# Optimization experiments

Hardware: AMD Instinct MI355X
Metric: run time of the kernel (lower is better)

Reference implementation:

```python
import jax, jax.numpy as jnp
import numpy as np

B, LC, LQ, D = 256, 400, 50, 128
NEG = 1e12


def setup_inputs() -> dict:
    key = jax.random.key(0)
    ks = jax.random.split(key, 7)
    return {
        "x_cont": jax.random.normal(ks[0], (B, LC, D), dtype=jnp.float32),
        "x_ques": jax.random.normal(ks[1], (B, LQ, D), dtype=jnp.float32),
        "W0": jax.random.normal(ks[2], (D, 1), dtype=jnp.float32) * (1.0 / np.sqrt(D)),
        "W1": jax.random.normal(ks[3], (D, 1), dtype=jnp.float32) * (1.0 / np.sqrt(D)),
        "W2": jax.random.normal(ks[4], (1, 1, D), dtype=jnp.float32) * (1.0 / np.sqrt(D)),
        "cont_len": jax.random.randint(ks[5], (B, 1), 1, LC, dtype=jnp.int32),
        "ques_len": jax.random.randint(ks[6], (B, 1), 1, LQ, dtype=jnp.int32),
    }


def reference(x_cont, x_ques, W0, W1, W2, cont_len, ques_len):
    # Trilinear similarity S[b,c,q] = xc.W0 + xq.W1 + (xc*W2).xq
    s_c = x_cont @ W0                                   # (B, LC, 1)
    s_q = jnp.swapaxes(x_ques @ W1, 1, 2)               # (B, 1, LQ)
    s_f = jnp.einsum('bcd,bqd->bcq', x_cont * W2, x_ques)
    S = s_c + s_q + s_f                                 # (B, LC, LQ)

    # Length masks: position valid iff pos < seq_len (matches one_hot+cumsum)
    q_mask = (jnp.arange(LQ)[None, :] < ques_len).astype(S.dtype)  # (B, LQ)
    c_mask = (jnp.arange(LC)[None, :] < cont_len).astype(S.dtype)  # (B, LC)

    S_bar = jax.nn.softmax(S - (1.0 - q_mask)[:, None, :] * NEG, axis=-1)
    S_T = jnp.swapaxes(
        jax.nn.softmax(S - (1.0 - c_mask)[:, :, None] * NEG, axis=1), 1, 2)  # (B, LQ, LC)

    c2q = S_bar @ x_ques                                # (B, LC, D)
    q2c = (S_bar @ S_T) @ x_cont                        # (B, LC, D)

    result = jnp.concatenate(
        [x_cont, c2q, x_cont * c2q, x_cont * q2c], axis=-1)  # (B, LC, 4D)
    return result, S_bar, S_T
```

## Files before the change

kernel.cpp:

```cpp
#include <hip/hip_runtime.h>
#include <math.h>

#define B 256
#define LC 400
#define LQ 50
#define D 128

#define CT 64
__global__ __launch_bounds__(256) void k_scores(
    const float* __restrict__ xc_g, const float* __restrict__ xq_g,
    const float* __restrict__ W0, const float* __restrict__ W1,
    const float* __restrict__ W2, float* __restrict__ S_raw)
{
    __shared__ __align__(16) float xq[56 * 132];
    __shared__ __align__(16) float xc[CT * 132];
    __shared__ float w[3 * D];
    __shared__ float sc[CT], sq[64];
    __shared__ float sS[CT * 51];

    const int b = blockIdx.y;
    const int c0 = blockIdx.x * CT;
    const int t = threadIdx.x;
    const int nc = min(CT, LC - c0);

    const float* xqb = xq_g + b * LQ * D;
    for (int i = t; i < LQ * D; i += 256) xq[(i >> 7) * 132 + (i & 127)] = xqb[i];
    const float* xcb = xc_g + (size_t)(b * LC + c0) * D;
    for (int i = t; i < nc * D; i += 256) xc[(i >> 7) * 132 + (i & 127)] = xcb[i];
    if (t < D) { w[t] = W0[t]; w[D + t] = W1[t]; w[2 * D + t] = W2[t]; }
    __syncthreads();

    if (t < nc) {
        const float4* r = (const float4*)(xc + t * 132);
        float4 a = {0.f, 0.f, 0.f, 0.f};
        const float4* wv = (const float4*)w;
        for (int d = 0; d < D / 4; ++d) {
            float4 u = r[d], vv = wv[d];
            a.x += u.x * vv.x; a.y += u.y * vv.y; a.z += u.z * vv.z; a.w += u.w * vv.w;
        }
        sc[t] = a.x + a.y + a.z + a.w;
    } else if (t >= 64 && t < 64 + LQ) {
        const int q = t - 64;
        const float4* r = (const float4*)(xq + q * 132);
        const float4* wv = (const float4*)(w + D);
        float4 a = {0.f, 0.f, 0.f, 0.f};
        for (int d = 0; d < D / 4; ++d) {
            float4 u = r[d], vv = wv[d];
            a.x += u.x * vv.x; a.y += u.y * vv.y; a.z += u.z * vv.z; a.w += u.w * vv.w;
        }
        sq[q] = a.x + a.y + a.z + a.w;
    }
    __syncthreads();
    for (int i = t; i < nc * D; i += 256) xc[(i >> 7) * 132 + (i & 127)] *= w[2 * D + (i & 127)];
    __syncthreads();

    const int qg = t & 7, cg = t >> 3;
    const int cA = cg * 2;
    if (cA < nc) {
        float accA[7] = {0, 0, 0, 0, 0, 0, 0};
        float accB[7] = {0, 0, 0, 0, 0, 0, 0};
        const float4* xc4 = (const float4*)xc;
        const float4* xq4 = (const float4*)xq;
#pragma unroll 8
        for (int d4 = 0; d4 < 32; ++d4) {
            const float4 a0 = xc4[cA * 33 + d4];
            const float4 a1 = xc4[(cA + 1) * 33 + d4];
#pragma unroll
            for (int j = 0; j < 7; ++j) {
                const float4 bq = xq4[(qg * 7 + j) * 33 + d4];
                accA[j] += a0.x * bq.x + a0.y * bq.y + a0.z * bq.z + a0.w * bq.w;
                accB[j] += a1.x * bq.x + a1.y * bq.y + a1.z * bq.z + a1.w * bq.w;
            }
        }
#pragma unroll
        for (int j = 0; j < 7; ++j) {
            const int q = qg * 7 + j;
            if (q < LQ) {
                sS[cA * 51 + q] = accA[j];
                sS[(cA + 1) * 51 + q] = accB[j];
            }
        }
    }
    __syncthreads();

    float* Sb = S_raw + (size_t)(b * LC + c0) * LQ;
    for (int i = t; i < nc * LQ; i += 256) {
        const int c = i / LQ, q = i % LQ;
        Sb[i] = sS[c * 51 + q] + sc[c] + sq[q];
    }
}

__global__ __launch_bounds__(512) void k_softmax_fused(
    float* S_inout, const int* __restrict__ cont_len,
    const int* __restrict__ ques_len, float* __restrict__ S_T)
{
    __shared__ float sS[LC * 53];
    __shared__ float red[512];
    __shared__ float colmax[64], colinv[64];
    __shared__ float rowmax[LC], rowinv[LC];

    const int b = blockIdx.x;
    const int t = threadIdx.x;
    const int clen = cont_len[b];
    const int qlen = ques_len[b];
    float* Sb = S_inout + (size_t)b * LC * LQ;

    for (int i = t; i < LC * LQ; i += 512) sS[(i / LQ) * 53 + (i % LQ)] = Sb[i];
    __syncthreads();

    const int q = t % LQ, r = t / LQ;
    if (r < 10) {
        float m = -INFINITY;
        const int cend = min((r + 1) * 40, clen);
        for (int c = r * 40; c < cend; ++c) m = fmaxf(m, sS[c * 53 + q]);
        red[r * LQ + q] = m;
    }
    __syncthreads();
    if (t < LQ) {
        float m = red[t];
        for (int rr = 1; rr < 10; ++rr) m = fmaxf(m, red[rr * LQ + t]);
        colmax[t] = m;
    }
    __syncthreads();
    if (r < 10) {
        float s = 0.f;
        const float cm = colmax[q];
        const int cend = min((r + 1) * 40, clen);
        for (int c = r * 40; c < cend; ++c) s += __expf(sS[c * 53 + q] - cm);
        red[r * LQ + q] = s;
    }
    __syncthreads();
    if (t < LQ) {
        float s = 0.f;
        for (int rr = 0; rr < 10; ++rr) s += red[rr * LQ + t];
        colinv[t] = 1.f / s;
    }
    if (t < LC) {
        float m = -INFINITY;
        for (int qq = 0; qq < qlen; ++qq) m = fmaxf(m, sS[t * 53 + qq]);
        float s = 0.f;
        for (int qq = 0; qq < qlen; ++qq) s += __expf(sS[t * 53 + qq] - m);
        rowmax[t] = m;
        rowinv[t] = 1.f / s;
    }
    __syncthreads();

    for (int i = t; i < LC * LQ; i += 512) {
        const int c = i / LQ, qq = i % LQ;
        const float v = (qq < qlen) ? __expf(sS[c * 53 + qq] - rowmax[c]) * rowinv[c] : 0.f;
        Sb[i] = v;
    }
    float* STb = S_T + (size_t)b * LQ * LC;
    for (int i = t; i < LQ * LC; i += 512) {
        const int qq = i / LC, c = i % LC;
        const float v = (c < clen) ? __expf(sS[c * 53 + qq] - colmax[qq]) * colinv[qq] : 0.f;
        STb[i] = v;
    }
}

__global__ __launch_bounds__(256) void k_qc(
    const float* __restrict__ S_T, const float* __restrict__ xc_g,
    float* __restrict__ T)
{
    __shared__ __align__(16) float sT[56 * 404];

    const int b = blockIdx.x;
    const int t = threadIdx.x;
    const float* STb = S_T + (size_t)b * LQ * LC;
    for (int i = t; i < LQ * LC; i += 256) sT[(i / LC) * 404 + (i % LC)] = STb[i];
    __syncthreads();

    const int d4 = t & 31, qg = t >> 5;
    float4 acc[7];
#pragma unroll
    for (int j = 0; j < 7; ++j) acc[j] = make_float4(0.f, 0.f, 0.f, 0.f);

    const float4* xcv = (const float4*)xc_g + (size_t)b * LC * 32 + d4;
    const float4* sT4 = (const float4*)sT;
    for (int c = 0; c < LC; c += 4) {
        const float4 x0 = xcv[(c + 0) * 32];
        const float4 x1 = xcv[(c + 1) * 32];
        const float4 x2 = xcv[(c + 2) * 32];
        const float4 x3 = xcv[(c + 3) * 32];
#pragma unroll
        for (int j = 0; j < 7; ++j) {
            const float4 wv = sT4[(qg * 7 + j) * 101 + (c >> 2)];
            acc[j].x += wv.x * x0.x + wv.y * x1.x + wv.z * x2.x + wv.w * x3.x;
            acc[j].y += wv.x * x0.y + wv.y * x1.y + wv.z * x2.y + wv.w * x3.y;
            acc[j].z += wv.x * x0.z + wv.y * x1.z + wv.z * x2.z + wv.w * x3.z;
            acc[j].w += wv.x * x0.w + wv.y * x1.w + wv.z * x2.w + wv.w * x3.w;
        }
    }
    float4* Tb = (float4*)T + (size_t)b * LQ * 32 + d4;
#pragma unroll
    for (int j = 0; j < 7; ++j) {
        const int qq = qg * 7 + j;
        if (qq < LQ) Tb[qq * 32] = acc[j];
    }
}

__global__ __launch_bounds__(256) void k_out(
    const float* __restrict__ S_bar, const float* __restrict__ xq_g,
    const float* __restrict__ Tm, const float* __restrict__ xc_g,
    float* __restrict__ out)
{
    __shared__ __align__(16) float xqL[LQ * 132];
    __shared__ __align__(16) float TL[LQ * 132];
    __shared__ float sbL[CT * 51];

    const int b = blockIdx.y;
    const int c0 = blockIdx.x * CT;
    const int t = threadIdx.x;
    const int nc = min(CT, LC - c0);

    const float* xqb = xq_g + (size_t)b * LQ * D;
    const float* Tb = Tm + (size_t)b * LQ * D;
    for (int i = t; i < LQ * D; i += 256) {
        xqL[(i >> 7) * 132 + (i & 127)] = xqb[i];
        TL[(i >> 7) * 132 + (i & 127)] = Tb[i];
    }
    const float* sb_g = S_bar + (size_t)(b * LC + c0) * LQ;
    for (int i = t; i < nc * LQ; i += 256) sbL[(i / LQ) * 51 + (i % LQ)] = sb_g[i];
    __syncthreads();

    const int d4 = t & 31, cg = t >> 5;
    float4 c2q[8], q2c[8];
#pragma unroll
    for (int i = 0; i < 8; ++i) {
        c2q[i] = make_float4(0.f, 0.f, 0.f, 0.f);
        q2c[i] = make_float4(0.f, 0.f, 0.f, 0.f);
    }
    const float4* xq4 = (const float4*)xqL;
    const float4* T4 = (const float4*)TL;
    const int cbase = cg * 8;
    for (int qq = 0; qq < LQ; ++qq) {
        const float4 xv = xq4[qq * 33 + d4];
        const float4 tv = T4[qq * 33 + d4];
#pragma unroll
        for (int i = 0; i < 8; ++i) {
            const float wq = sbL[(cbase + i) * 51 + qq];
            c2q[i].x += wq * xv.x; c2q[i].y += wq * xv.y;
            c2q[i].z += wq * xv.z; c2q[i].w += wq * xv.w;
            q2c[i].x += wq * tv.x; q2c[i].y += wq * tv.y;
            q2c[i].z += wq * tv.z; q2c[i].w += wq * tv.w;
        }
    }

    const float4* xcv = (const float4*)xc_g;
    float4* out4 = (float4*)out;
#pragma unroll
    for (int i = 0; i < 8; ++i) {
        const int c = cbase + i;
        if (c < nc) {
            const int row = b * LC + c0 + c;
            const float4 xc = xcv[(size_t)row * 32 + d4];
            float4* o = out4 + (size_t)row * 128 + d4;
            o[0] = xc;
            o[32] = c2q[i];
            o[64] = make_float4(xc.x * c2q[i].x, xc.y * c2q[i].y,
                                xc.z * c2q[i].z, xc.w * c2q[i].w);
            o[96] = make_float4(xc.x * q2c[i].x, xc.y * q2c[i].y,
                                xc.z * q2c[i].z, xc.w * q2c[i].w);
        }
    }
}

extern "C" void kernel_launch(void* const* d_in, const int* in_sizes, int n_in,
                              void* d_out, int out_size, void* d_ws, size_t ws_size,
                              hipStream_t stream)
{
    (void)in_sizes; (void)n_in; (void)out_size; (void)ws_size;
    const float* x_cont = (const float*)d_in[0];
    const float* x_ques = (const float*)d_in[1];
    const float* W0 = (const float*)d_in[2];
    const float* W1 = (const float*)d_in[3];
    const float* W2 = (const float*)d_in[4];
    const int* cont_len = (const int*)d_in[5];
    const int* ques_len = (const int*)d_in[6];

    float* out = (float*)d_out;
    float* out_res  = out;
    float* out_Sbar = out + (size_t)B * LC * 4 * D;
    float* out_ST   = out_Sbar + (size_t)B * LC * LQ;
    float* Tws = (float*)d_ws;

    k_scores<<<dim3(7, B), 256, 0, stream>>>(x_cont, x_ques, W0, W1, W2, out_Sbar);
    k_softmax_fused<<<B, 512, 0, stream>>>(out_Sbar, cont_len, ques_len, out_ST);
    k_qc<<<B, 256, 0, stream>>>(out_ST, x_cont, Tws);
    k_out<<<dim3(7, B), 256, 0, stream>>>(out_Sbar, x_ques, Tws, x_cont, out_res);
}
```

Measured before the change: 439.8 us.

## Fuse score computation with softmax into one per-batch kernel and vectorize loads

Merges the score kernel and the softmax kernel into a single block per batch. It tiles over context rows in shared memory and prefetches the next tile into registers, so raw scores never round-trip through global memory and one launch is removed. The W2 scaling moves from the context rows to the question matrix. It also vectorizes the S_T staging load in k_qc and transposes S_bar in shared memory in k_out so weights can be read as float4. The trade-off is much less grid parallelism for the score stage (256 blocks, only half the threads doing the main product) and higher shared-memory use per block.

```diff
diff --git a/kernel.cpp b/kernel.cpp
--- a/kernel.cpp
+++ b/kernel.cpp
@@ -5,156 +5,184 @@
 #define LC 400
 #define LQ 50
 #define D 128
-
 #define CT 64
-__global__ __launch_bounds__(256) void k_scores(
+
+__global__ __launch_bounds__(256) void k_scores_softmax(
     const float* __restrict__ xc_g, const float* __restrict__ xq_g,
     const float* __restrict__ W0, const float* __restrict__ W1,
-    const float* __restrict__ W2, float* __restrict__ S_raw)
+    const float* __restrict__ W2, const int* __restrict__ cont_len,
+    const int* __restrict__ ques_len,
+    float* __restrict__ S_bar, float* __restrict__ S_T)
 {
+    __shared__ float sS[LC * 51];
     __shared__ __align__(16) float xq[56 * 132];
-    __shared__ __align__(16) float xc[CT * 132];
+    __shared__ __align__(16) float xc[64 * 132];
     __shared__ float w[3 * D];
-    __shared__ float sc[CT], sq[64];
-    __shared__ float sS[CT * 51];
-
-    const int b = blockIdx.y;
-    const int c0 = blockIdx.x * CT;
-    const int t = threadIdx.x;
-    const int nc = min(CT, LC - c0);
-
-    const float* xqb = xq_g + b * LQ * D;
-    for (int i = t; i < LQ * D; i += 256) xq[(i >> 7) * 132 + (i & 127)] = xqb[i];
-    const float* xcb = xc_g + (size_t)(b * LC + c0) * D;
-    for (int i = t; i < nc * D; i += 256) xc[(i >> 7) * 132 + (i & 127)] = xcb[i];
-    if (t < D) { w[t] = W0[t]; w[D + t] = W1[t]; w[2 * D + t] = W2[t]; }
-    __syncthreads();
-
-    if (t < nc) {
-        const float4* r = (const float4*)(xc + t * 132);
-        float4 a = {0.f, 0.f, 0.f, 0.f};
-        const float4* wv = (const float4*)w;
-        for (int d = 0; d < D / 4; ++d) {
-            float4 u = r[d], vv = wv[d];
-            a.x += u.x * vv.x; a.y += u.y * vv.y; a.z += u.z * vv.z; a.w += u.w * vv.w;
-        }
-        sc[t] = a.x + a.y + a.z + a.w;
-    } else if (t >= 64 && t < 64 + LQ) {
-        const int q = t - 64;
-        const float4* r = (const float4*)(xq + q * 132);
-        const float4* wv = (const float4*)(w + D);
-        float4 a = {0.f, 0.f, 0.f, 0.f};
-        for (int d = 0; d < D / 4; ++d) {
-            float4 u = r[d], vv = wv[d];
-            a.x += u.x * vv.x; a.y += u.y * vv.y; a.z += u.z * vv.z; a.w += u.w * vv.w;
-        }
-        sq[q] = a.x + a.y + a.z + a.w;
-    }
-    __syncthreads();
-    for (int i = t; i < nc * D; i += 256) xc[(i >> 7) * 132 + (i & 127)] *= w[2 * D + (i & 127)];
-    __syncthreads();
-
-    const int qg = t & 7, cg = t >> 3;
-    const int cA = cg * 2;
-    if (cA < nc) {
-        float accA[7] = {0, 0, 0, 0, 0, 0, 0};
-        float accB[7] = {0, 0, 0, 0, 0, 0, 0};
-        const float4* xc4 = (const float4*)xc;
-        const float4* xq4 = (const float4*)xq;
-#pragma unroll 8
-        for (int d4 = 0; d4 < 32; ++d4) {
-            const float4 a0 = xc4[cA * 33 + d4];
-            const float4 a1 = xc4[(cA + 1) * 33 + d4];
-#pragma unroll
-            for (int j = 0; j < 7; ++j) {
-                const float4 bq = xq4[(qg * 7 + j) * 33 + d4];
-                accA[j] += a0.x * bq.x + a0.y * bq.y + a0.z * bq.z + a0.w * bq.w;
-                accB[j] += a1.x * bq.x + a1.y * bq.y + a1.z * bq.z + a1.w * bq.w;
-            }
-        }
-#pragma unroll
-        for (int j = 0; j < 7; ++j) {
-            const int q = qg * 7 + j;
-            if (q < LQ) {
-                sS[cA * 51 + q] = accA[j];
-                sS[(cA + 1) * 51 + q] = accB[j];
-            }
-        }
-    }
-    __syncthreads();
-
-    float* Sb = S_raw + (size_t)(b * LC + c0) * LQ;
-    for (int i = t; i < nc * LQ; i += 256) {
-        const int c = i / LQ, q = i % LQ;
-        Sb[i] = sS[c * 51 + q] + sc[c] + sq[q];
-    }
-}
-
-__global__ __launch_bounds__(512) void k_softmax_fused(
-    float* S_inout, const int* __restrict__ cont_len,
-    const int* __restrict__ ques_len, float* __restrict__ S_T)
-{
-    __shared__ float sS[LC * 53];
-    __shared__ float red[512];
-    __shared__ float colmax[64], colinv[64];
+    __shared__ float scT[64];
+    __shared__ float sq[56];
     __shared__ float rowmax[LC], rowinv[LC];
+    __shared__ float colmax[LQ], colinv[LQ];
+    __shared__ float red[256];
 
     const int b = blockIdx.x;
     const int t = threadIdx.x;
     const int clen = cont_len[b];
     const int qlen = ques_len[b];
-    float* Sb = S_inout + (size_t)b * LC * LQ;
-
-    for (int i = t; i < LC * LQ; i += 512) sS[(i / LQ) * 53 + (i % LQ)] = Sb[i];
-    __syncthreads();
-
-    const int q = t % LQ, r = t / LQ;
-    if (r < 10) {
+
+    const float4* xq4g = (const float4*)(xq_g + (size_t)b * LQ * D);
+    for (int i = t; i < LQ * 32; i += 256)
+        ((float4*)xq)[(i >> 5) * 33 + (i & 31)] = xq4g[i];
+    {
+        const float4* g0 = (const float4*)(xc_g + (size_t)b * LC * D);
+        for (int i = t; i < 64 * 32; i += 256)
+            ((float4*)xc)[(i >> 5) * 33 + (i & 31)] = g0[i];
+    }
+    if (t < D) { w[t] = W0[t]; w[D + t] = W1[t]; w[2 * D + t] = W2[t]; }
+    __syncthreads();
+
+    if (t < LQ) {
+        const float4* r = (const float4*)(xq + t * 132);
+        const float4* wv = (const float4*)(w + D);
+        float4 a = {0.f, 0.f, 0.f, 0.f};
+#pragma unroll
+        for (int d = 0; d < 32; ++d) {
+            float4 u = r[d], v = wv[d];
+            a.x += u.x * v.x; a.y += u.y * v.y; a.z += u.z * v.z; a.w += u.w * v.w;
+        }
+        sq[t] = a.x + a.y + a.z + a.w;
+    }
+    __syncthreads();
+    for (int i = t; i < LQ * D; i += 256)
+        xq[(i >> 7) * 132 + (i & 127)] *= w[2 * D + (i & 127)];
+    __syncthreads();
+
+    const int qg = t & 7;
+    const int cg = (t >> 3) & 15;
+
+    for (int tile = 0; tile < 7; ++tile) {
+        const int c0 = tile * 64;
+        const int nc = min(64, LC - c0);
+
+        float4 pf[8];
+        const int c0n = c0 + 64;
+        const int ncn = (tile < 6) ? min(64, LC - c0n) : 0;
+        const float4* gn = (const float4*)(xc_g + ((size_t)b * LC + c0n) * D);
+#pragma unroll
+        for (int k = 0; k < 8; ++k) {
+            const int i = t + k * 256;
+            if (i < ncn * 32) pf[k] = gn[i];
+        }
+
+        float acc[4][7];
+        if (t < 128) {
+#pragma unroll
+            for (int i = 0; i < 4; ++i)
+#pragma unroll
+                for (int j = 0; j < 7; ++j) acc[i][j] = 0.f;
+            const float4* xc4 = (const float4*)xc;
+            const float4* xq4 = (const float4*)xq;
+#pragma unroll 4
+            for (int d4 = 0; d4 < 32; ++d4) {
+                const float4 a0 = xc4[(cg + 0)  * 33 + d4];
+                const float4 a1 = xc4[(cg + 16) * 33 + d4];
+                const float4 a2 = xc4[(cg + 32) * 33 + d4];
+                const float4 a3 = xc4[(cg + 48) * 33 + d4];
+#pragma unroll
+                for (int j = 0; j < 7; ++j) {
+                    const float4 bq = xq4[(qg * 7 + j) * 33 + d4];
+                    acc[0][j] += a0.x*bq.x + a0.y*bq.y + a0.z*bq.z + a0.w*bq.w;
+                    acc[1][j] += a1.x*bq.x + a1.y*bq.y + a1.z*bq.z + a1.w*bq.w;
+                    acc[2][j] += a2.x*bq.x + a2.y*bq.y + a2.z*bq.z + a2.w*bq.w;
+                    acc[3][j] += a3.x*bq.x + a3.y*bq.y + a3.z*bq.z + a3.w*bq.w;
+                }
+            }
+        } else if (t < 192) {
+            const int c = t - 128;
+            if (c < nc) {
+                const float4* r = (const float4*)(xc + c * 132);
+                const float4* wv = (const float4*)w;
+                float4 a = {0.f, 0.f, 0.f, 0.f};
+#pragma unroll
+                for (int d = 0; d < 32; ++d) {
+                    float4 u = r[d], v = wv[d];
+                    a.x += u.x*v.x; a.y += u.y*v.y; a.z += u.z*v.z; a.w += u.w*v.w;
+                }
+                scT[c] = a.x + a.y + a.z + a.w;
+            }
+        }
+        __syncthreads();
+
+        if (t < 128) {
+#pragma unroll
+            for (int i = 0; i < 4; ++i) {
+                const int c = cg + 16 * i;
+                if (c < nc) {
+                    const float sc_c = scT[c];
+#pragma unroll
+                    for (int j = 0; j < 7; ++j) {
+                        const int q = qg * 7 + j;
+                        if (q < LQ) sS[(c0 + c) * 51 + q] = acc[i][j] + sc_c + sq[q];
+                    }
+                }
+            }
+        }
+#pragma unroll
+        for (int k = 0; k < 8; ++k) {
+            const int i = t + k * 256;
+            if (i < ncn * 32) ((float4*)xc)[(i >> 5) * 33 + (i & 31)] = pf[k];
+        }
+        __syncthreads();
+    }
+
+    const int qq_ = t % LQ;
+    const int r_ = t / LQ;
+    if (t < 250) {
         float m = -INFINITY;
-        const int cend = min((r + 1) * 40, clen);
-        for (int c = r * 40; c < cend; ++c) m = fmaxf(m, sS[c * 53 + q]);
-        red[r * LQ + q] = m;
+        const int ce = min((r_ + 1) * 80, clen);
+        for (int c = r_ * 80; c < ce; ++c) m = fmaxf(m, sS[c * 51 + qq_]);
+        red[t] = m;
     }
     __syncthreads();
     if (t < LQ) {
         float m = red[t];
-        for (int rr = 1; rr < 10; ++rr) m = fmaxf(m, red[rr * LQ + t]);
+#pragma unroll
+        for (int rr = 1; rr < 5; ++rr) m = fmaxf(m, red[rr * LQ + t]);
         colmax[t] = m;
     }
     __syncthreads();
-    if (r < 10) {
+    if (t < 250) {
         float s = 0.f;
-        const float cm = colmax[q];
-        const int cend = min((r + 1) * 40, clen);
-        for (int c = r * 40; c < cend; ++c) s += __expf(sS[c * 53 + q] - cm);
-        red[r * LQ + q] = s;
+        const float cm = colmax[qq_];
+        const int ce = min((r_ + 1) * 80, clen);
+        for (int c = r_ * 80; c < ce; ++c) s += __expf(sS[c * 51 + qq_] - cm);
+        red[t] = s;
     }
     __syncthreads();
     if (t < LQ) {
+        float s = red[t];
+#pragma unroll
+        for (int rr = 1; rr < 5; ++rr) s += red[rr * LQ + t];
+        colinv[t] = 1.f / s;
+    }
+    for (int c = t; c < LC; c += 256) {
+        float m = -INFINITY;
+        for (int q = 0; q < qlen; ++q) m = fmaxf(m, sS[c * 51 + q]);
         float s = 0.f;
-        for (int rr = 0; rr < 10; ++rr) s += red[rr * LQ + t];
-        colinv[t] = 1.f / s;
-    }
-    if (t < LC) {
-        float m = -INFINITY;
-        for (int qq = 0; qq < qlen; ++qq) m = fmaxf(m, sS[t * 53 + qq]);
-        float s = 0.f;
-        for (int qq = 0; qq < qlen; ++qq) s += __expf(sS[t * 53 + qq] - m);
-        rowmax[t] = m;
-        rowinv[t] = 1.f / s;
-    }
-    __syncthreads();
-
-    for (int i = t; i < LC * LQ; i += 512) {
-        const int c = i / LQ, qq = i % LQ;
-        const float v = (qq < qlen) ? __expf(sS[c * 53 + qq] - rowmax[c]) * rowinv[c] : 0.f;
-        Sb[i] = v;
+        for (int q = 0; q < qlen; ++q) s += __expf(sS[c * 51 + q] - m);
+        rowmax[c] = m;
+        rowinv[c] = 1.f / s;
+    }
+    __syncthreads();
+
+    float* Sb = S_bar + (size_t)b * LC * LQ;
+    for (int i = t; i < LC * LQ; i += 256) {
+        const int c = i / LQ, q = i - c * LQ;
+        Sb[i] = (q < qlen) ? __expf(sS[c * 51 + q] - rowmax[c]) * rowinv[c] : 0.f;
     }
     float* STb = S_T + (size_t)b * LQ * LC;
-    for (int i = t; i < LQ * LC; i += 512) {
-        const int qq = i / LC, c = i % LC;
-        const float v = (c < clen) ? __expf(sS[c * 53 + qq] - colmax[qq]) * colinv[qq] : 0.f;
-        STb[i] = v;
+    for (int i = t; i < LQ * LC; i += 256) {
+        const int q = i / LC, c = i - q * LC;
+        STb[i] = (c < clen) ? __expf(sS[c * 51 + q] - colmax[q]) * colinv[q] : 0.f;
     }
 }
 
@@ -166,8 +194,10 @@
 
     const int b = blockIdx.x;
     const int t = threadIdx.x;
-    const float* STb = S_T + (size_t)b * LQ * LC;
-    for (int i = t; i < LQ * LC; i += 256) sT[(i / LC) * 404 + (i % LC)] = STb[i];
+    const float4* STb4 = (const float4*)(S_T + (size_t)b * LQ * LC);
+    float4* sTw = (float4*)sT;
+    for (int i = t; i < LQ * 100; i += 256)
+        sTw[(i / 100) * 101 + (i % 100)] = STb4[i];
     __syncthreads();
 
     const int d4 = t & 31, qg = t >> 5;
@@ -199,6 +229,8 @@
     }
 }
 
+#define FMA4(A, s, V) { A.x += (s) * V.x; A.y += (s) * V.y; A.z += (s) * V.z; A.w += (s) * V.w; }
+
 __global__ __launch_bounds__(256) void k_out(
     const float* __restrict__ S_bar, const float* __restrict__ xq_g,
     const float* __restrict__ Tm, const float* __restrict__ xc_g,
@@ -206,21 +238,25 @@
 {
     __shared__ __align__(16) float xqL[LQ * 132];
     __shared__ __align__(16) float TL[LQ * 132];
-    __shared__ float sbL[CT * 51];
+    __shared__ __align__(16) float sbT[LQ * 68];
 
     const int b = blockIdx.y;
     const int c0 = blockIdx.x * CT;
     const int t = threadIdx.x;
     const int nc = min(CT, LC - c0);
 
-    const float* xqb = xq_g + (size_t)b * LQ * D;
-    const float* Tb = Tm + (size_t)b * LQ * D;
-    for (int i = t; i < LQ * D; i += 256) {
-        xqL[(i >> 7) * 132 + (i & 127)] = xqb[i];
-        TL[(i >> 7) * 132 + (i & 127)] = Tb[i];
+    const float4* xq4g = (const float4*)(xq_g + (size_t)b * LQ * D);
+    const float4* T4g  = (const float4*)(Tm + (size_t)b * LQ * D);
+    for (int i = t; i < LQ * 32; i += 256) {
+        const int row = i >> 5, col = i & 31;
+        ((float4*)xqL)[row * 33 + col] = xq4g[i];
+        ((float4*)TL)[row * 33 + col]  = T4g[i];
     }
     const float* sb_g = S_bar + (size_t)(b * LC + c0) * LQ;
-    for (int i = t; i < nc * LQ; i += 256) sbL[(i / LQ) * 51 + (i % LQ)] = sb_g[i];
+    for (int i = t; i < nc * LQ; i += 256) {
+        const int c = i / LQ, q = i - c * LQ;
+        sbT[q * 68 + c] = sb_g[i];
+    }
     __syncthreads();
 
     const int d4 = t & 31, cg = t >> 5;
@@ -231,21 +267,25 @@
         q2c[i] = make_float4(0.f, 0.f, 0.f, 0.f);
     }
     const float4* xq4 = (const float4*)xqL;
-    const float4* T4 = (const float4*)TL;
-    const int cbase = cg * 8;
+    const float4* T4  = (const float4*)TL;
+    const float4* sb4 = (const float4*)sbT;
+    const int cb2 = cg * 2;
     for (int qq = 0; qq < LQ; ++qq) {
         const float4 xv = xq4[qq * 33 + d4];
         const float4 tv = T4[qq * 33 + d4];
-#pragma unroll
-        for (int i = 0; i < 8; ++i) {
-            const float wq = sbL[(cbase + i) * 51 + qq];
-            c2q[i].x += wq * xv.x; c2q[i].y += wq * xv.y;
-            c2q[i].z += wq * xv.z; c2q[i].w += wq * xv.w;
-            q2c[i].x += wq * tv.x; q2c[i].y += wq * tv.y;
-            q2c[i].z += wq * tv.z; q2c[i].w += wq * tv.w;
-        }
-    }
-
+        const float4 s0 = sb4[qq * 17 + cb2];
+        const float4 s1 = sb4[qq * 17 + cb2 + 1];
+        FMA4(c2q[0], s0.x, xv); FMA4(q2c[0], s0.x, tv);
+        FMA4(c2q[1], s0.y, xv); FMA4(q2c[1], s0.y, tv);
+        FMA4(c2q[2], s0.z, xv); FMA4(q2c[2], s0.z, tv);
+        FMA4(c2q[3], s0.w, xv); FMA4(q2c[3], s0.w, tv);
+        FMA4(c2q[4], s1.x, xv); FMA4(q2c[4], s1.x, tv);
+        FMA4(c2q[5], s1.y, xv); FMA4(q2c[5], s1.y, tv);
+        FMA4(c2q[6], s1.z, xv); FMA4(q2c[6], s1.z, tv);
+        FMA4(c2q[7], s1.w, xv); FMA4(q2c[7], s1.w, tv);
+    }
+
+    const int cbase = cg * 8;
     const float4* xcv = (const float4*)xc_g;
     float4* out4 = (float4*)out;
 #pragma unroll
@@ -284,8 +324,8 @@
     float* out_ST   = out_Sbar + (size_t)B * LC * LQ;
     float* Tws = (float*)d_ws;
 
-    k_scores<<<dim3(7, B), 256, 0, stream>>>(x_cont, x_ques, W0, W1, W2, out_Sbar);
-    k_softmax_fused<<<B, 512, 0, stream>>>(out_Sbar, cont_len, ques_len, out_ST);
+    k_scores_softmax<<<B, 256, 0, stream>>>(x_cont, x_ques, W0, W1, W2,
+                                            cont_len, ques_len, out_Sbar, out_ST);
     k_qc<<<B, 256, 0, stream>>>(out_ST, x_cont, Tws);
     k_out<<<dim3(7, B), 256, 0, stream>>>(out_Sbar, x_ques, Tws, x_cont, out_res);
 }
```

Measured after the change: 520.7 us. 18.4% more time.
